# Kernel optimization log

Hardware: AMD Instinct MI355X
Metric: run time of the kernel (lower is better)

The kernel has to match this reference:

```python
import jax, jax.numpy as jnp
import numpy as np

NUM_HEADS = 16
SLICE_SIZE = 1024
SCALING = SLICE_SIZE ** 0.5  # module divides by sqrt(slice_size), as written


def setup_inputs() -> dict:
    key = jax.random.key(0)
    ks = jax.random.split(key, 9)
    B, S, D = 4, 2048, SLICE_SIZE
    sc = 0.02
    return {
        "x": jax.random.normal(ks[0], (B, S, D), dtype=jnp.float32),
        "Wq": jax.random.normal(ks[1], (D, D), dtype=jnp.float32) * sc,
        "bq": jax.random.normal(ks[2], (D,), dtype=jnp.float32) * sc,
        "Wk": jax.random.normal(ks[3], (D, D), dtype=jnp.float32) * sc,
        "bk": jax.random.normal(ks[4], (D,), dtype=jnp.float32) * sc,
        "Wv": jax.random.normal(ks[5], (D, D), dtype=jnp.float32) * sc,
        "bv": jax.random.normal(ks[6], (D,), dtype=jnp.float32) * sc,
        "Wp": jax.random.normal(ks[7], (D, D), dtype=jnp.float32) * sc,
        "bp": jax.random.normal(ks[8], (D,), dtype=jnp.float32) * sc,
    }


def _split_heads(t):
    # 'b s (h o) -> b h s o'
    b, s, d = t.shape
    return t.reshape(b, s, NUM_HEADS, d // NUM_HEADS).transpose(0, 2, 1, 3)


def reference(x, Wq, bq, Wk, bk, Wv, bv, Wp, bp):
    q = _split_heads(x @ Wq.T + bq)  # [B,H,S,O]
    k = _split_heads(x @ Wk.T + bk)
    v = _split_heads(x @ Wv.T + bv)
    energy = jnp.einsum('bhqo,bhko->bhqk', q, k)  # full score matrix
    attn = jax.nn.softmax(energy / SCALING, axis=-1)
    # Faithful to source: 'b h q k, b h v o -> b h v o' sums attn over (q,k)
    out = jnp.einsum('bhqk,bhvo->bhvo', attn, v)
    b, h, s, o = out.shape
    out = out.transpose(0, 2, 1, 3).reshape(b, s, h * o)  # 'b h v o -> b v (h o)'
    return out @ Wp.T + bp
```

## Files before the change

### kernel.cpp

```cpp
#include <hip/hip_runtime.h>
#include <cstdint>


typedef unsigned short u16;
typedef __bf16 bf16x8 __attribute__((ext_vector_type(8)));
typedef float f32x4 __attribute__((ext_vector_type(4)));

__device__ __forceinline__ u16 f2bf(float f) {
  unsigned int u = __float_as_uint(f);
  u += 0x7fffu + ((u >> 16) & 1u);
  return (u16)(u >> 16);
}

__device__ __forceinline__ void load16(const void* g, void* l) {
  auto gp = (const __attribute__((address_space(1))) unsigned int*)(uintptr_t)g;
  auto lp = (__attribute__((address_space(3))) unsigned int*)(unsigned int)(uintptr_t)l;
  __builtin_amdgcn_global_load_lds(gp, lp, 16, 0, 0);
}

__global__ void k_prep(const float* __restrict__ x, const float* __restrict__ Wv,
                       const float* __restrict__ bv, const float* __restrict__ Wp,
                       const float* __restrict__ bp, u16* __restrict__ xb,
                       u16* __restrict__ wpb, u16* __restrict__ wvtb,
                       float* __restrict__ cv) {
  __shared__ float tile[32][33];
  const int b = blockIdx.x;
  const int tid = threadIdx.x;
  if (b < 9216) {
    const float* src = (b < 8192) ? x : Wp;
    u16* dst = (b < 8192) ? xb : wpb;
    const long base = (long)((b < 8192) ? b : (b - 8192)) * 1024 + tid * 4;
    const float4 v = *(const float4*)(src + base);
    ushort4 o;
    o.x = f2bf(v.x); o.y = f2bf(v.y); o.z = f2bf(v.z); o.w = f2bf(v.w);
    *(ushort4*)(dst + base) = o;
  } else if (b < 10240) {
    const int tb = b - 9216;
    const int bi = (tb & 31) * 32;
    const int bj = (tb >> 5) * 32;
    const int tx = tid & 31;
    const int ty = tid >> 5;
    for (int r = ty; r < 32; r += 8)
      tile[r][tx] = Wv[(long)(bj + r) * 1024 + bi + tx];
    __syncthreads();
    for (int r = ty; r < 32; r += 8)
      wvtb[(long)(bi + r) * 1024 + bj + tx] = f2bf(tile[tx][r]);
  } else {
    const int row = (b - 10240) * 4 + (tid >> 6);
    const int lane = tid & 63;
    const float* w = Wp + (long)row * 1024;
    float s = 0.f;
    for (int j = lane; j < 1024; j += 64) s += w[j] * bv[j];
    for (int off = 32; off; off >>= 1) s += __shfl_down(s, off, 64);
    if (lane == 0) cv[row] = 2048.f * s + bp[row];
  }
}

__global__ __launch_bounds__(256) void k_gemm0(
    const u16* __restrict__ A, const u16* __restrict__ B, float* __restrict__ Out,
    const float* __restrict__ bias, int M, int N, int K) {
  __shared__ u16 As[2][128 * 32];
  __shared__ u16 Bs[2][64 * 32];

  const int tid = threadIdx.x;
  const int lane = tid & 63;
  const int wv = tid >> 6;
  const int waveM = (wv & 1) << 6;
  const int waveN = (wv >> 1) << 5;
  const int l15 = lane & 15;
  const int quad = lane >> 4;

  const int id = blockIdx.x;
  const int xcd = id & 7;
  const int j = id >> 3;
  const long bm = (long)(xcd * 8 + (j >> 4)) * 128;
  const long bn = (long)(j & 15) * 64;

  const int rl = lane >> 2;
  const int cs = (lane & 3) ^ ((lane >> 3) & 3);
  const u16* Ag0 = A + (bm + wv * 16 + rl) * (long)K + cs * 8;
  const u16* Bg0 = B + (bn + wv * 16 + rl) * (long)K + cs * 8;
  const long rowOff = 64 * (long)K;

  const int nT = K >> 5;

  auto STAGE = [&](long k0, int b) {
    u16* Ad = &As[b][0] + (wv << 9);
    u16* Bd = &Bs[b][0] + (wv << 9);
    load16(Ag0 + k0, Ad);
    load16(Ag0 + rowOff + k0, Ad + 2048);
    load16(Bg0 + k0, Bd);
  };

  const f32x4 zero = {0.f, 0.f, 0.f, 0.f};
  f32x4 acc[4][2];
#pragma unroll
  for (int i = 0; i < 4; ++i)
#pragma unroll
    for (int j2 = 0; j2 < 2; ++j2) acc[i][j2] = zero;

  const int rq = quad ^ ((l15 >> 1) & 3);

  STAGE(0, 0);
  asm volatile("s_waitcnt vmcnt(0)" ::: "memory");
  __builtin_amdgcn_s_barrier();

  int cur = 0;
  for (int t = 0; t < nT; ++t) {
    const bool more = (t + 1) < nT;
    if (more) STAGE((long)(t + 1) << 5, cur ^ 1);
    __builtin_amdgcn_sched_barrier(0);

    const u16* Asb = &As[cur][0];
    const u16* Bsb = &Bs[cur][0];
    bf16x8 af[4], bg[2];
#pragma unroll
    for (int i = 0; i < 4; ++i)
      af[i] = *(const bf16x8*)(Asb + (waveM + i * 16 + l15) * 32 + rq * 8);
#pragma unroll
    for (int j2 = 0; j2 < 2; ++j2)
      bg[j2] = *(const bf16x8*)(Bsb + (waveN + j2 * 16 + l15) * 32 + rq * 8);
    asm volatile("s_waitcnt lgkmcnt(0)" ::: "memory");
    __builtin_amdgcn_sched_barrier(0);

#pragma unroll
    for (int i = 0; i < 4; ++i)
#pragma unroll
      for (int j2 = 0; j2 < 2; ++j2)
        acc[i][j2] = __builtin_amdgcn_mfma_f32_16x16x32_bf16(af[i], bg[j2],
                                                             acc[i][j2], 0, 0, 0);

    if (more) {
      asm volatile("s_waitcnt vmcnt(0)" ::: "memory");
      __builtin_amdgcn_s_barrier();
      cur ^= 1;
    }
  }

#pragma unroll
  for (int i = 0; i < 4; ++i) {
    const long gm = bm + waveM + i * 16 + quad * 4;
#pragma unroll
    for (int j2 = 0; j2 < 2; ++j2) {
      const long gn = bn + waveN + j2 * 16 + l15;
      const float bb = bias[gn];
#pragma unroll
      for (int r = 0; r < 4; ++r)
        Out[(gm + r) * N + gn] = acc[i][j2][r] + bb;
    }
  }
}

__global__ __launch_bounds__(256) void k_gemm1(
    const u16* __restrict__ A, const u16* __restrict__ B, u16* __restrict__ Out,
    int M, int N, int K) {
  __shared__ u16 As[2][64 * 64];
  __shared__ u16 Bs[2][64 * 64];

  const int tid = threadIdx.x;
  const int lane = tid & 63;
  const int wv = tid >> 6;
  const int waveM = (wv & 1) << 5;
  const int waveN = (wv >> 1) << 5;
  const int l15 = lane & 15;
  const int quad = lane >> 4;

  const long bm = (long)(blockIdx.x >> 4) * 64;
  const long bn = (long)(blockIdx.x & 15) * 64;

  const int rl = tid >> 3;
  const int cs = (tid & 7) ^ (rl & 7);
  const u16* Ag0 = A + (bm + rl) * (long)K + cs * 8;
  const u16* Bg0 = B + (bn + rl) * (long)K + cs * 8;
  constexpr int RPC = 32;

  const int nT = K >> 6;

  auto STAGE = [&](long k0, int b) {
    u16* Ad = &As[b][0] + tid * 8;
    u16* Bd = &Bs[b][0] + tid * 8;
    load16(Ag0 + k0, Ad);
    load16(Ag0 + k0 + (long)RPC * K, Ad + RPC * 64);
    load16(Bg0 + k0, Bd);
    load16(Bg0 + k0 + (long)RPC * K, Bd + RPC * 64);
  };

  const f32x4 zero = {0.f, 0.f, 0.f, 0.f};
  f32x4 acc[2][2];
#pragma unroll
  for (int i = 0; i < 2; ++i)
#pragma unroll
    for (int j = 0; j < 2; ++j) acc[i][j] = zero;

  const int rq0 = quad ^ (l15 & 7);
  const int rq1 = (4 + quad) ^ (l15 & 7);

  STAGE(0, 0);
  asm volatile("s_waitcnt vmcnt(0)" ::: "memory");
  __builtin_amdgcn_s_barrier();

  int cur = 0;
  for (int t = 0; t < nT; ++t) {
    const bool more = (t + 1) < nT;
    if (more) STAGE((long)(t + 1) << 6, cur ^ 1);
    __builtin_amdgcn_sched_barrier(0);

    const u16* Asb = &As[cur][0];
    const u16* Bsb = &Bs[cur][0];
    bf16x8 af[2][2], bg[2][2];
#pragma unroll
    for (int i = 0; i < 2; ++i) {
      const int ra = (waveM + i * 16 + l15) * 64;
      af[0][i] = *(const bf16x8*)(Asb + ra + rq0 * 8);
      af[1][i] = *(const bf16x8*)(Asb + ra + rq1 * 8);
    }
#pragma unroll
    for (int j = 0; j < 2; ++j) {
      const int rb = (waveN + j * 16 + l15) * 64;
      bg[0][j] = *(const bf16x8*)(Bsb + rb + rq0 * 8);
      bg[1][j] = *(const bf16x8*)(Bsb + rb + rq1 * 8);
    }
    asm volatile("s_waitcnt lgkmcnt(0)" ::: "memory");
    __builtin_amdgcn_sched_barrier(0);

#pragma unroll
    for (int kk = 0; kk < 2; ++kk)
#pragma unroll
      for (int i = 0; i < 2; ++i)
#pragma unroll
        for (int j = 0; j < 2; ++j)
          acc[i][j] = __builtin_amdgcn_mfma_f32_16x16x32_bf16(af[kk][i], bg[kk][j],
                                                              acc[i][j], 0, 0, 0);

    if (more) {
      asm volatile("s_waitcnt vmcnt(0)" ::: "memory");
      __builtin_amdgcn_s_barrier();
      cur ^= 1;
    }
  }

#pragma unroll
  for (int i = 0; i < 2; ++i) {
    const long gm = bm + waveM + i * 16 + quad * 4;
#pragma unroll
    for (int j = 0; j < 2; ++j) {
      const long gn = bn + waveN + j * 16 + l15;
#pragma unroll
      for (int r = 0; r < 4; ++r)
        Out[(gm + r) * N + gn] = f2bf(acc[i][j][r] * 2048.f);
    }
  }
}

extern "C" void kernel_launch(void* const* d_in, const int* in_sizes, int n_in,
                              void* d_out, int out_size, void* d_ws, size_t ws_size,
                              hipStream_t stream) {
  const float* x  = (const float*)d_in[0];
  const float* Wv = (const float*)d_in[5];
  const float* bv = (const float*)d_in[6];
  const float* Wp = (const float*)d_in[7];
  const float* bp = (const float*)d_in[8];

  char* ws = (char*)d_ws;
  u16* xb    = (u16*)(ws);
  u16* wpb   = (u16*)(ws + (16u << 20));
  u16* wvtb  = (u16*)(ws + (18u << 20));
  u16* m2b   = (u16*)(ws + (20u << 20));
  float* cv  = (float*)(ws + (22u << 20));

  k_prep<<<10496, 256, 0, stream>>>(x, Wv, bv, Wp, bp, xb, wpb, wvtb, cv);

  k_gemm1<<<256, 256, 0, stream>>>(wpb, wvtb, m2b, 1024, 1024, 1024);

  k_gemm0<<<1024, 256, 0, stream>>>(xb, m2b, (float*)d_out, cv,
                                    8192, 1024, 1024);
}
```

Before: 147.9 us.

## Retile output GEMM to 256x128 blocks with triple-buffered LDS pipeline

Rewrites the main x·M GEMM kernel to use 512-thread blocks computing 256x128 tiles with a K-step of 64. Global-to-LDS loads run through a three-stage ring buffer, with each stage's loads split between two half-iterations. MFMA phases are wrapped in s_setprio to favour the math. The aim is more data reuse per block and better overlap of loads with compute. The grid shrinks to one block per CU. It uses about 147KB of LDS and hardcodes the problem sizes, which risks low occupancy and no tail tolerance.

```diff
diff --git a/kernel.cpp b/kernel.cpp
--- a/kernel.cpp
+++ b/kernel.cpp
@@ -56,97 +56,143 @@
   }
 }
 
-__global__ __launch_bounds__(256) void k_gemm0(
+__global__ __launch_bounds__(512) void k_gemm0(
     const u16* __restrict__ A, const u16* __restrict__ B, float* __restrict__ Out,
-    const float* __restrict__ bias, int M, int N, int K) {
-  __shared__ u16 As[2][128 * 32];
-  __shared__ u16 Bs[2][64 * 32];
+    const float* __restrict__ bias) {
+  __shared__ u16 As[3][256 * 64];
+  __shared__ u16 Bs[3][128 * 64];
 
   const int tid = threadIdx.x;
   const int lane = tid & 63;
   const int wv = tid >> 6;
-  const int waveM = (wv & 1) << 6;
-  const int waveN = (wv >> 1) << 5;
+  const int waveM = (wv & 1) * 128;
+  const int waveN = (wv >> 1) * 32;
   const int l15 = lane & 15;
   const int quad = lane >> 4;
 
   const int id = blockIdx.x;
   const int xcd = id & 7;
   const int j = id >> 3;
-  const long bm = (long)(xcd * 8 + (j >> 4)) * 128;
-  const long bn = (long)(j & 15) * 64;
-
-  const int rl = lane >> 2;
-  const int cs = (lane & 3) ^ ((lane >> 3) & 3);
-  const u16* Ag0 = A + (bm + wv * 16 + rl) * (long)K + cs * 8;
-  const u16* Bg0 = B + (bn + wv * 16 + rl) * (long)K + cs * 8;
-  const long rowOff = 64 * (long)K;
-
-  const int nT = K >> 5;
-
-  auto STAGE = [&](long k0, int b) {
-    u16* Ad = &As[b][0] + (wv << 9);
-    u16* Bd = &Bs[b][0] + (wv << 9);
-    load16(Ag0 + k0, Ad);
-    load16(Ag0 + rowOff + k0, Ad + 2048);
-    load16(Bg0 + k0, Bd);
+  const long bm = (long)(xcd * 4 + (j >> 3)) * 256;
+  const long bn = (long)(j & 7) * 128;
+
+  const int rl = tid >> 3;
+  const int cs = (tid & 7) ^ (rl & 7);
+  const u16* Ag = A + (bm + rl) * 1024L + cs * 8;
+  const u16* Bg = B + (bn + rl) * 1024L + cs * 8;
+
+  auto STAGE_A = [&](int tt, int r) {
+    u16* d = &As[tt % 3][0] + r * 4096 + tid * 8;
+    load16(Ag + ((long)tt << 6) + (long)r * 64 * 1024, d);
   };
+  auto STAGE_B = [&](int tt, int r) {
+    u16* d = &Bs[tt % 3][0] + r * 4096 + tid * 8;
+    load16(Bg + ((long)tt << 6) + (long)r * 64 * 1024, d);
+  };
 
   const f32x4 zero = {0.f, 0.f, 0.f, 0.f};
-  f32x4 acc[4][2];
-#pragma unroll
-  for (int i = 0; i < 4; ++i)
-#pragma unroll
-    for (int j2 = 0; j2 < 2; ++j2) acc[i][j2] = zero;
-
-  const int rq = quad ^ ((l15 >> 1) & 3);
-
-  STAGE(0, 0);
-  asm volatile("s_waitcnt vmcnt(0)" ::: "memory");
+  f32x4 acc[8][2];
+#pragma unroll
+  for (int i = 0; i < 8; ++i)
+#pragma unroll
+    for (int jj = 0; jj < 2; ++jj) acc[i][jj] = zero;
+
+  const int rq0 = quad ^ (l15 & 7);
+  const int rq1 = (4 + quad) ^ (l15 & 7);
+
+  constexpr int nT = 16;
+
+#pragma unroll
+  for (int r = 0; r < 4; ++r) STAGE_A(0, r);
+  STAGE_B(0, 0); STAGE_B(0, 1);
+#pragma unroll
+  for (int r = 0; r < 4; ++r) STAGE_A(1, r);
+  STAGE_B(1, 0); STAGE_B(1, 1);
+  asm volatile("s_waitcnt vmcnt(6)" ::: "memory");
   __builtin_amdgcn_s_barrier();
 
-  int cur = 0;
   for (int t = 0; t < nT; ++t) {
-    const bool more = (t + 1) < nT;
-    if (more) STAGE((long)(t + 1) << 5, cur ^ 1);
-    __builtin_amdgcn_sched_barrier(0);
-
-    const u16* Asb = &As[cur][0];
-    const u16* Bsb = &Bs[cur][0];
-    bf16x8 af[4], bg[2];
-#pragma unroll
-    for (int i = 0; i < 4; ++i)
-      af[i] = *(const bf16x8*)(Asb + (waveM + i * 16 + l15) * 32 + rq * 8);
-#pragma unroll
-    for (int j2 = 0; j2 < 2; ++j2)
-      bg[j2] = *(const bf16x8*)(Bsb + (waveN + j2 * 16 + l15) * 32 + rq * 8);
-    asm volatile("s_waitcnt lgkmcnt(0)" ::: "memory");
-    __builtin_amdgcn_sched_barrier(0);
-
-#pragma unroll
-    for (int i = 0; i < 4; ++i)
-#pragma unroll
-      for (int j2 = 0; j2 < 2; ++j2)
-        acc[i][j2] = __builtin_amdgcn_mfma_f32_16x16x32_bf16(af[i], bg[j2],
-                                                             acc[i][j2], 0, 0, 0);
-
-    if (more) {
-      asm volatile("s_waitcnt vmcnt(0)" ::: "memory");
-      __builtin_amdgcn_s_barrier();
-      cur ^= 1;
-    }
-  }
-
-#pragma unroll
-  for (int i = 0; i < 4; ++i) {
+    const u16* Asb = &As[t % 3][0];
+    const u16* Bsb = &Bs[t % 3][0];
+    const bool st = (t + 2) < nT;
+
+    {
+      bf16x8 af[2][4], bg[2][2];
+#pragma unroll
+      for (int i = 0; i < 4; ++i) {
+        const int ra = (waveM + i * 16 + l15) * 64;
+        af[0][i] = *(const bf16x8*)(Asb + ra + rq0 * 8);
+        af[1][i] = *(const bf16x8*)(Asb + ra + rq1 * 8);
+      }
+#pragma unroll
+      for (int jj = 0; jj < 2; ++jj) {
+        const int rb = (waveN + jj * 16 + l15) * 64;
+        bg[0][jj] = *(const bf16x8*)(Bsb + rb + rq0 * 8);
+        bg[1][jj] = *(const bf16x8*)(Bsb + rb + rq1 * 8);
+      }
+      if (st) { STAGE_A(t + 2, 0); STAGE_A(t + 2, 1); STAGE_A(t + 2, 2); }
+      __builtin_amdgcn_sched_barrier(0);
+      __builtin_amdgcn_s_barrier();
+      asm volatile("s_waitcnt lgkmcnt(0)" ::: "memory");
+      __builtin_amdgcn_sched_barrier(0);
+      __builtin_amdgcn_s_setprio(1);
+#pragma unroll
+      for (int kk = 0; kk < 2; ++kk)
+#pragma unroll
+        for (int i = 0; i < 4; ++i)
+#pragma unroll
+          for (int jj = 0; jj < 2; ++jj)
+            acc[i][jj] = __builtin_amdgcn_mfma_f32_16x16x32_bf16(
+                af[kk][i], bg[kk][jj], acc[i][jj], 0, 0, 0);
+      __builtin_amdgcn_s_setprio(0);
+      __builtin_amdgcn_s_barrier();
+    }
+
+    {
+      bf16x8 af[2][4], bg[2][2];
+#pragma unroll
+      for (int i = 0; i < 4; ++i) {
+        const int ra = (waveM + 64 + i * 16 + l15) * 64;
+        af[0][i] = *(const bf16x8*)(Asb + ra + rq0 * 8);
+        af[1][i] = *(const bf16x8*)(Asb + ra + rq1 * 8);
+      }
+#pragma unroll
+      for (int jj = 0; jj < 2; ++jj) {
+        const int rb = (waveN + jj * 16 + l15) * 64;
+        bg[0][jj] = *(const bf16x8*)(Bsb + rb + rq0 * 8);
+        bg[1][jj] = *(const bf16x8*)(Bsb + rb + rq1 * 8);
+      }
+      if (st) { STAGE_A(t + 2, 3); STAGE_B(t + 2, 0); STAGE_B(t + 2, 1); }
+      __builtin_amdgcn_sched_barrier(0);
+      __builtin_amdgcn_s_barrier();
+      asm volatile("s_waitcnt lgkmcnt(0)" ::: "memory");
+      __builtin_amdgcn_sched_barrier(0);
+      __builtin_amdgcn_s_setprio(1);
+#pragma unroll
+      for (int kk = 0; kk < 2; ++kk)
+#pragma unroll
+        for (int i = 0; i < 4; ++i)
+#pragma unroll
+          for (int jj = 0; jj < 2; ++jj)
+            acc[4 + i][jj] = __builtin_amdgcn_mfma_f32_16x16x32_bf16(
+                af[kk][i], bg[kk][jj], acc[4 + i][jj], 0, 0, 0);
+      __builtin_amdgcn_s_setprio(0);
+      if (st)                asm volatile("s_waitcnt vmcnt(6)" ::: "memory");
+      else if (t + 1 < nT)   asm volatile("s_waitcnt vmcnt(0)" ::: "memory");
+      __builtin_amdgcn_s_barrier();
+    }
+  }
+
+#pragma unroll
+  for (int i = 0; i < 8; ++i) {
     const long gm = bm + waveM + i * 16 + quad * 4;
 #pragma unroll
-    for (int j2 = 0; j2 < 2; ++j2) {
-      const long gn = bn + waveN + j2 * 16 + l15;
+    for (int jj = 0; jj < 2; ++jj) {
+      const long gn = bn + waveN + jj * 16 + l15;
       const float bb = bias[gn];
 #pragma unroll
       for (int r = 0; r < 4; ++r)
-        Out[(gm + r) * N + gn] = acc[i][j2][r] + bb;
+        Out[(gm + r) * 1024 + gn] = acc[i][jj][r] + bb;
     }
   }
 }
@@ -272,6 +318,5 @@
 
   k_gemm1<<<256, 256, 0, stream>>>(wpb, wvtb, m2b, 1024, 1024, 1024);
 
-  k_gemm0<<<1024, 256, 0, stream>>>(xb, m2b, (float*)d_out, cv,
-                                    8192, 1024, 1024);
-}
+  k_gemm0<<<256, 512, 0, stream>>>(xb, m2b, (float*)d_out, cv);
+}
```

Result: faster. 143.4 us (-3.0%).
